# Optimization experiments

Measured on AMD Instinct MI355X. Metric: run time of the kernel, lower is better.

The kernel has to match this reference:

```python
import jax, jax.numpy as jnp
import numpy as np

EPS = 0.0  # init eps


def setup_inputs() -> dict:
    key = jax.random.key(0)
    k1, k2 = jax.random.split(key)
    features = jax.random.normal(k1, (8, 64, 100000), dtype=jnp.float32)
    coords = jax.random.normal(k2, (8, 3, 100000), dtype=jnp.float32)
    return {"features": features, "coords": coords, "resolution": 32}


def _voxelize(features, coords, r):
    # coords: [B, 3, N], features: [B, C, N]
    coords = jax.lax.stop_gradient(coords)  # original does coords.detach()
    norm_coords = coords - jnp.mean(coords, axis=2, keepdims=True)
    # normalize=True branch: divide by 2*max point radius, shift to [0,1]
    radius = jnp.linalg.norm(norm_coords, axis=1, keepdims=True)        # [B,1,N]
    scale = jnp.max(radius, axis=2, keepdims=True) * 2.0 + EPS          # [B,1,1]
    norm_coords = norm_coords / scale + 0.5
    norm_coords = jnp.clip(norm_coords * r, 0, r - 1)                   # [B,3,N]
    vox = jnp.round(norm_coords).astype(jnp.int32)                      # [B,3,N]

    B, C, N = features.shape
    flat_idx = (vox[:, 0] * r + vox[:, 1]) * r + vox[:, 2]              # [B,N]
    seg_ids = (flat_idx + jnp.arange(B, dtype=jnp.int32)[:, None] * (r ** 3)).reshape(-1)

    feats = jnp.transpose(features, (0, 2, 1)).reshape(B * N, C)        # [B*N,C]
    sums = jax.ops.segment_sum(feats, seg_ids, num_segments=B * r ** 3)  # [B*r^3,C]
    cnts = jax.ops.segment_sum(jnp.ones((B * N,), features.dtype), seg_ids,
                               num_segments=B * r ** 3)                  # [B*r^3]
    avg = sums / jnp.maximum(cnts, 1.0)[:, None]
    vox_feat = jnp.transpose(avg.reshape(B, r ** 3, C), (0, 2, 1)).reshape(B, C, r, r, r)
    return vox_feat, norm_coords


def reference(features, coords, resolution):
    return _voxelize(features, coords, int(resolution))
```

## Files before the change

kernel.cpp:

```cpp
#include <hip/hip_runtime.h>
#include <math.h>

static constexpr int B = 8;
static constexpr int C = 64;
static constexpr int N = 100000;
static constexpr int RES = 32;
static constexpr int R3 = RES * RES * RES;
static constexpr int NQ = N / 4;

static constexpr int   SCALE_BITS = 19;
static constexpr float FSCALE     = (float)(1 << SCALE_BITS);
static constexpr float INV_FSCALE = 1.0f / FSCALE;

typedef float vfloat4 __attribute__((ext_vector_type(4)));

static constexpr size_t MEANP_OFF = 0;
static constexpr size_t MAXP_OFF  = 1536;
static constexpr size_t CNT_OFF   = 2048;
static constexpr size_t VID_OFF   = CNT_OFF + (size_t)B * R3 * sizeof(int);

__device__ __forceinline__ int vhash(int v) { return v ^ (v >> 5) ^ (v >> 10); }

__device__ __forceinline__ double block_reduce_sum(double v) {
    for (int off = 32; off > 0; off >>= 1) v += __shfl_down(v, off, 64);
    __shared__ double s[4];
    int lane = threadIdx.x & 63, w = threadIdx.x >> 6;
    if (lane == 0) s[w] = v;
    __syncthreads();
    if (threadIdx.x == 0) v = (s[0] + s[1]) + (s[2] + s[3]);
    return v;
}

__device__ __forceinline__ float block_reduce_max(float v) {
    for (int off = 32; off > 0; off >>= 1) v = fmaxf(v, __shfl_down(v, off, 64));
    __shared__ float s[4];
    int lane = threadIdx.x & 63, w = threadIdx.x >> 6;
    if (lane == 0) s[w] = v;
    __syncthreads();
    if (threadIdx.x == 0) v = fmaxf(fmaxf(s[0], s[1]), fmaxf(s[2], s[3]));
    return v;
}

__global__ void k_mean(const float* __restrict__ coords, double* __restrict__ mean_part,
                       int* __restrict__ cnt) {
    int gtid = blockIdx.x * blockDim.x + threadIdx.x;
    int4* c4 = (int4*)cnt;
    for (int i = gtid; i < B * R3 / 4; i += gridDim.x * blockDim.x)
        c4[i] = make_int4(0, 0, 0, 0);

    const int NSLICE = 8;
    int pair  = blockIdx.x % (B * 3);
    int slice = blockIdx.x / (B * 3);
    const float* p = coords + (size_t)pair * N;
    double acc = 0.0;
#pragma unroll 4
    for (int i = slice * 256 + threadIdx.x; i < N; i += NSLICE * 256)
        acc += (double)p[i];
    acc = block_reduce_sum(acc);
    if (threadIdx.x == 0) mean_part[pair * 8 + slice] = acc;
}

__global__ void k_max(const float* __restrict__ coords,
                      const double* __restrict__ mean_part,
                      float* __restrict__ max_part) {
    const int NSLICE = 16;
    int b     = blockIdx.x % B;
    int slice = blockIdx.x / B;
    __shared__ float sm[3];
    if (threadIdx.x < 3) {
        double s = 0.0;
#pragma unroll
        for (int k = 0; k < 8; ++k) s += mean_part[(b * 3 + threadIdx.x) * 8 + k];
        sm[threadIdx.x] = (float)(s / (double)N);
    }
    __syncthreads();
    float mx = sm[0], my = sm[1], mz = sm[2];
    const float4* px = (const float4*)(coords + (size_t)(b * 3 + 0) * N);
    const float4* py = (const float4*)(coords + (size_t)(b * 3 + 1) * N);
    const float4* pz = (const float4*)(coords + (size_t)(b * 3 + 2) * N);
    float m = 0.0f;
    for (int i = slice * 256 + threadIdx.x; i < NQ; i += NSLICE * 256) {
        float4 x4 = px[i], y4 = py[i], z4 = pz[i];
        float x, y, z;
        x = x4.x - mx; y = y4.x - my; z = z4.x - mz; m = fmaxf(m, x*x + y*y + z*z);
        x = x4.y - mx; y = y4.y - my; z = z4.y - mz; m = fmaxf(m, x*x + y*y + z*z);
        x = x4.z - mx; y = y4.z - my; z = z4.z - mz; m = fmaxf(m, x*x + y*y + z*z);
        x = x4.w - mx; y = y4.w - my; z = z4.w - mz; m = fmaxf(m, x*x + y*y + z*z);
    }
    m = block_reduce_max(m);
    if (threadIdx.x == 0) max_part[b * 16 + slice] = m;
}

__global__ __launch_bounds__(256) void k_vid(const float* __restrict__ coords,
                      const double* __restrict__ mean_part,
                      const float* __restrict__ max_part,
                      unsigned short* __restrict__ vid,
                      float* __restrict__ out_norm) {
    int b = blockIdx.y;
    __shared__ float sm[4];
    if (threadIdx.x < 3) {
        double s = 0.0;
#pragma unroll
        for (int k = 0; k < 8; ++k) s += mean_part[(b * 3 + threadIdx.x) * 8 + k];
        sm[threadIdx.x] = (float)(s / (double)N);
    }
    if (threadIdx.x == 3) {
        float m = max_part[b * 16];
#pragma unroll
        for (int k = 1; k < 16; ++k) m = fmaxf(m, max_part[b * 16 + k]);
        sm[3] = 2.0f * sqrtf(m);
    }
    __syncthreads();
    int q = blockIdx.x * 256 + threadIdx.x;
    if (q >= NQ) return;
    float m0 = sm[0], m1 = sm[1], m2 = sm[2], scale = sm[3];

    const float4* p0 = (const float4*)(coords + (size_t)(b * 3 + 0) * N);
    const float4* p1 = (const float4*)(coords + (size_t)(b * 3 + 1) * N);
    const float4* p2 = (const float4*)(coords + (size_t)(b * 3 + 2) * N);
    float4* o0 = (float4*)(out_norm + (size_t)(b * 3 + 0) * N);
    float4* o1 = (float4*)(out_norm + (size_t)(b * 3 + 1) * N);
    float4* o2 = (float4*)(out_norm + (size_t)(b * 3 + 2) * N);
    float4 x4 = p0[q], y4 = p1[q], z4 = p2[q];

#define NORM1(v, mm) { v = (v - mm) / scale + 0.5f; v = v * (float)RES;     \
                       v = fminf(fmaxf(v, 0.0f), (float)(RES - 1)); }
    NORM1(x4.x, m0); NORM1(x4.y, m0); NORM1(x4.z, m0); NORM1(x4.w, m0);
    NORM1(y4.x, m1); NORM1(y4.y, m1); NORM1(y4.z, m1); NORM1(y4.w, m1);
    NORM1(z4.x, m2); NORM1(z4.y, m2); NORM1(z4.z, m2); NORM1(z4.w, m2);
#undef NORM1
    o0[q] = x4; o1[q] = y4; o2[q] = z4;

    int f0 = ((int)rintf(x4.x) * RES + (int)rintf(y4.x)) * RES + (int)rintf(z4.x);
    int f1 = ((int)rintf(x4.y) * RES + (int)rintf(y4.y)) * RES + (int)rintf(z4.y);
    int f2 = ((int)rintf(x4.z) * RES + (int)rintf(y4.z)) * RES + (int)rintf(z4.z);
    int f3 = ((int)rintf(x4.w) * RES + (int)rintf(y4.w)) * RES + (int)rintf(z4.w);
    ushort4 h;
    h.x = (unsigned short)vhash(f0); h.y = (unsigned short)vhash(f1);
    h.z = (unsigned short)vhash(f2); h.w = (unsigned short)vhash(f3);
    ((ushort4*)(vid + (size_t)b * N))[q] = h;
}

__global__ __launch_bounds__(1024) void k_cnt(const unsigned short* __restrict__ vid,
                                              int* __restrict__ cnt) {
    extern __shared__ char smem[];
    int* grid = (int*)smem;
    const int b = blockIdx.x & 7, slice = blockIdx.x >> 3, tid = threadIdx.x;
    constexpr int QS = NQ / 4;
    int4* g4 = (int4*)grid;
    for (int i = tid; i < R3 / 4; i += 1024) g4[i] = make_int4(0, 0, 0, 0);
    __syncthreads();
    const uint2* vp = (const uint2*)(vid + (size_t)b * N);
    for (int i = slice * QS + tid; i < (slice + 1) * QS; i += 1024) {
        uint2 v = vp[i];
        atomicAdd(&grid[(int)(v.x & 0xffffu)], 1);
        atomicAdd(&grid[(int)(v.x >> 16)],     1);
        atomicAdd(&grid[(int)(v.y & 0xffffu)], 1);
        atomicAdd(&grid[(int)(v.y >> 16)],     1);
    }
    __syncthreads();
    int* cb = cnt + (size_t)b * R3;
    for (int i = tid; i < R3; i += 1024) {
        int v = grid[vhash(i)];
        if (v) atomicAdd(&cb[i], v);
    }
}

__global__ __launch_bounds__(1024, 4) void k_accum(const unsigned short* __restrict__ vid,
                                                   const float* __restrict__ feats,
                                                   const int* __restrict__ cnt,
                                                   float* __restrict__ out_vox) {
    extern __shared__ char smem[];
    int* grid = (int*)smem;
    constexpr int BS = 1024, U = 6, STEP = BS * U;
    constexpr int NITER = 4;
    constexpr int NMAIN = NITER * STEP;
    int b = blockIdx.x & 7;
    int c = blockIdx.x >> 3;
    const uint2*   vp = (const uint2*)(vid + (size_t)b * N);
    const vfloat4* fp = (const vfloat4*)(feats + ((size_t)(b * C + c)) * N);
    const int tid = threadIdx.x;

    uint2 vA[U], vB[U]; vfloat4 fA[U], fB[U];

#define LOADC(dstv, dstf, chunk)                                            \
    {   int _base = (chunk) * STEP + tid;                                   \
        _Pragma("unroll")                                                   \
        for (int u = 0; u < U; ++u) {                                       \
            dstv[u] = vp[_base + u * BS];                                   \
            dstf[u] = __builtin_nontemporal_load(&fp[_base + u * BS]);      \
        } }
#define PROC(sv, sf)                                                        \
    {   _Pragma("unroll")                                                   \
        for (int u = 0; u < U; ++u) {                                       \
            uint2 vv = sv[u]; vfloat4 ff = sf[u];                           \
            atomicAdd(&grid[(int)(vv.x & 0xffffu)], __float2int_rn(ff.x * FSCALE)); \
            atomicAdd(&grid[(int)(vv.x >> 16)],     __float2int_rn(ff.y * FSCALE)); \
            atomicAdd(&grid[(int)(vv.y & 0xffffu)], __float2int_rn(ff.z * FSCALE)); \
            atomicAdd(&grid[(int)(vv.y >> 16)],     __float2int_rn(ff.w * FSCALE)); \
        } }

    LOADC(vA, fA, 0);
    LOADC(vB, fB, 1);
    int4* g4 = (int4*)grid;
    for (int i = tid; i < R3 / 4; i += BS) g4[i] = make_int4(0, 0, 0, 0);
    __syncthreads();

    __builtin_amdgcn_sched_barrier(0);
    PROC(vA, fA);
    LOADC(vA, fA, 2);
    __builtin_amdgcn_sched_barrier(0);
    PROC(vB, fB);
    LOADC(vB, fB, 3);
    __builtin_amdgcn_sched_barrier(0);
    PROC(vA, fA);
    __builtin_amdgcn_sched_barrier(0);
    PROC(vB, fB);
#undef LOADC
#undef PROC

    for (int i = NMAIN + tid; i < NQ; i += BS) {
        uint2 v = vp[i];
        vfloat4 f = __builtin_nontemporal_load(&fp[i]);
        atomicAdd(&grid[(int)(v.x & 0xffffu)], __float2int_rn(f.x * FSCALE));
        atomicAdd(&grid[(int)(v.x >> 16)],     __float2int_rn(f.y * FSCALE));
        atomicAdd(&grid[(int)(v.y & 0xffffu)], __float2int_rn(f.z * FSCALE));
        atomicAdd(&grid[(int)(v.y >> 16)],     __float2int_rn(f.w * FSCALE));
    }
    __syncthreads();

    const int4* cp4 = (const int4*)(cnt + (size_t)b * R3);
    vfloat4* op4 = (vfloat4*)(out_vox + ((size_t)(b * C + c)) * R3);
    for (int i = tid; i < R3 / 4; i += BS) {
        int4 c4v = cp4[i];
        int base = i * 4;
        vfloat4 o;
        o.x = ((float)grid[vhash(base + 0)] * INV_FSCALE) / fmaxf((float)c4v.x, 1.0f);
        o.y = ((float)grid[vhash(base + 1)] * INV_FSCALE) / fmaxf((float)c4v.y, 1.0f);
        o.z = ((float)grid[vhash(base + 2)] * INV_FSCALE) / fmaxf((float)c4v.z, 1.0f);
        o.w = ((float)grid[vhash(base + 3)] * INV_FSCALE) / fmaxf((float)c4v.w, 1.0f);
        __builtin_nontemporal_store(o, &op4[i]);
    }
}

extern "C" void kernel_launch(void* const* d_in, const int* in_sizes, int n_in,
                              void* d_out, int out_size, void* d_ws, size_t ws_size,
                              hipStream_t stream) {
    const float* feats  = (const float*)d_in[0];
    const float* coords = (const float*)d_in[1];
    float* out_vox  = (float*)d_out;
    float* out_norm = out_vox + (size_t)B * C * R3;

    double*         mean_part = (double*)((char*)d_ws + MEANP_OFF);
    float*          max_part  = (float*)((char*)d_ws + MAXP_OFF);
    int*            cnt       = (int*)((char*)d_ws + CNT_OFF);
    unsigned short* vid       = (unsigned short*)((char*)d_ws + VID_OFF);

    static bool attr_done = false;
    if (!attr_done) {
        (void)hipFuncSetAttribute((const void*)k_accum,
                            hipFuncAttributeMaxDynamicSharedMemorySize, R3 * sizeof(int));
        (void)hipFuncSetAttribute((const void*)k_cnt,
                            hipFuncAttributeMaxDynamicSharedMemorySize, R3 * sizeof(int));
        attr_done = true;
    }

    k_mean<<<B * 3 * 8, 256, 0, stream>>>(coords, mean_part, cnt);
    k_max<<<B * 16, 256, 0, stream>>>(coords, mean_part, max_part);
    k_vid<<<dim3((NQ + 255) / 256, B), 256, 0, stream>>>(coords, mean_part, max_part,
                                                         vid, out_norm);
    k_cnt<<<B * 4, 1024, R3 * sizeof(int), stream>>>(vid, cnt);
    k_accum<<<B * C, 1024, R3 * sizeof(int), stream>>>(vid, feats, cnt, out_vox);
}
```

Measured before the change: 319.6 us.

## Precompute reciprocal counts, retune accum pipeline depth, nontemporal norm stores

Adds a small kernel that turns per-voxel counts into reciprocals in place, so the 512 accumulation blocks multiply instead of dividing in their epilogue. The accumulation loop changes from 4 chunks of 6 vectors per thread to 6 chunks of 4, which lowers register pressure while keeping the double-buffered prefetch. Normalized coordinate stores become nontemporal. The cost is one extra kernel launch, and results can differ slightly because multiplying by a reciprocal rounds differently from a true divide.

```diff
diff --git a/kernel.cpp b/kernel.cpp
--- a/kernel.cpp
+++ b/kernel.cpp
@@ -118,9 +118,9 @@
     const float4* p0 = (const float4*)(coords + (size_t)(b * 3 + 0) * N);
     const float4* p1 = (const float4*)(coords + (size_t)(b * 3 + 1) * N);
     const float4* p2 = (const float4*)(coords + (size_t)(b * 3 + 2) * N);
-    float4* o0 = (float4*)(out_norm + (size_t)(b * 3 + 0) * N);
-    float4* o1 = (float4*)(out_norm + (size_t)(b * 3 + 1) * N);
-    float4* o2 = (float4*)(out_norm + (size_t)(b * 3 + 2) * N);
+    vfloat4* o0 = (vfloat4*)(out_norm + (size_t)(b * 3 + 0) * N);
+    vfloat4* o1 = (vfloat4*)(out_norm + (size_t)(b * 3 + 1) * N);
+    vfloat4* o2 = (vfloat4*)(out_norm + (size_t)(b * 3 + 2) * N);
     float4 x4 = p0[q], y4 = p1[q], z4 = p2[q];
 
 #define NORM1(v, mm) { v = (v - mm) / scale + 0.5f; v = v * (float)RES;     \
@@ -129,7 +129,12 @@
     NORM1(y4.x, m1); NORM1(y4.y, m1); NORM1(y4.z, m1); NORM1(y4.w, m1);
     NORM1(z4.x, m2); NORM1(z4.y, m2); NORM1(z4.z, m2); NORM1(z4.w, m2);
 #undef NORM1
-    o0[q] = x4; o1[q] = y4; o2[q] = z4;
+    vfloat4 vx = {x4.x, x4.y, x4.z, x4.w};
+    vfloat4 vy = {y4.x, y4.y, y4.z, y4.w};
+    vfloat4 vz = {z4.x, z4.y, z4.z, z4.w};
+    __builtin_nontemporal_store(vx, &o0[q]);
+    __builtin_nontemporal_store(vy, &o1[q]);
+    __builtin_nontemporal_store(vz, &o2[q]);
 
     int f0 = ((int)rintf(x4.x) * RES + (int)rintf(y4.x)) * RES + (int)rintf(z4.x);
     int f1 = ((int)rintf(x4.y) * RES + (int)rintf(y4.y)) * RES + (int)rintf(z4.y);
@@ -166,14 +171,25 @@
     }
 }
 
+__global__ __launch_bounds__(1024) void k_inv(int* __restrict__ cnt) {
+    int i = blockIdx.x * 1024 + threadIdx.x;
+    int4 v = ((const int4*)cnt)[i];
+    vfloat4 o;
+    o.x = 1.0f / fmaxf((float)v.x, 1.0f);
+    o.y = 1.0f / fmaxf((float)v.y, 1.0f);
+    o.z = 1.0f / fmaxf((float)v.z, 1.0f);
+    o.w = 1.0f / fmaxf((float)v.w, 1.0f);
+    ((vfloat4*)cnt)[i] = o;
+}
+
 __global__ __launch_bounds__(1024, 4) void k_accum(const unsigned short* __restrict__ vid,
                                                    const float* __restrict__ feats,
                                                    const int* __restrict__ cnt,
                                                    float* __restrict__ out_vox) {
     extern __shared__ char smem[];
     int* grid = (int*)smem;
-    constexpr int BS = 1024, U = 6, STEP = BS * U;
-    constexpr int NITER = 4;
+    constexpr int BS = 1024, U = 4, STEP = BS * U;
+    constexpr int NITER = 6;
     constexpr int NMAIN = NITER * STEP;
     int b = blockIdx.x & 7;
     int c = blockIdx.x >> 3;
@@ -214,6 +230,12 @@
     LOADC(vB, fB, 3);
     __builtin_amdgcn_sched_barrier(0);
     PROC(vA, fA);
+    LOADC(vA, fA, 4);
+    __builtin_amdgcn_sched_barrier(0);
+    PROC(vB, fB);
+    LOADC(vB, fB, 5);
+    __builtin_amdgcn_sched_barrier(0);
+    PROC(vA, fA);
     __builtin_amdgcn_sched_barrier(0);
     PROC(vB, fB);
 #undef LOADC
@@ -229,16 +251,16 @@
     }
     __syncthreads();
 
-    const int4* cp4 = (const int4*)(cnt + (size_t)b * R3);
+    const vfloat4* ip4 = (const vfloat4*)(cnt + (size_t)b * R3);
     vfloat4* op4 = (vfloat4*)(out_vox + ((size_t)(b * C + c)) * R3);
     for (int i = tid; i < R3 / 4; i += BS) {
-        int4 c4v = cp4[i];
+        vfloat4 iv = ip4[i];
         int base = i * 4;
         vfloat4 o;
-        o.x = ((float)grid[vhash(base + 0)] * INV_FSCALE) / fmaxf((float)c4v.x, 1.0f);
-        o.y = ((float)grid[vhash(base + 1)] * INV_FSCALE) / fmaxf((float)c4v.y, 1.0f);
-        o.z = ((float)grid[vhash(base + 2)] * INV_FSCALE) / fmaxf((float)c4v.z, 1.0f);
-        o.w = ((float)grid[vhash(base + 3)] * INV_FSCALE) / fmaxf((float)c4v.w, 1.0f);
+        o.x = ((float)grid[vhash(base + 0)] * INV_FSCALE) * iv.x;
+        o.y = ((float)grid[vhash(base + 1)] * INV_FSCALE) * iv.y;
+        o.z = ((float)grid[vhash(base + 2)] * INV_FSCALE) * iv.z;
+        o.w = ((float)grid[vhash(base + 3)] * INV_FSCALE) * iv.w;
         __builtin_nontemporal_store(o, &op4[i]);
     }
 }
@@ -270,5 +292,6 @@
     k_vid<<<dim3((NQ + 255) / 256, B), 256, 0, stream>>>(coords, mean_part, max_part,
                                                          vid, out_norm);
     k_cnt<<<B * 4, 1024, R3 * sizeof(int), stream>>>(vid, cnt);
+    k_inv<<<B * R3 / 4096, 1024, 0, stream>>>(cnt);
     k_accum<<<B * C, 1024, R3 * sizeof(int), stream>>>(vid, feats, cnt, out_vox);
 }
```

Result: no change. 316.2 us (-1.1%).
